# Performance work log

Hardware: AMD Instinct MI355X
Metric: run time of the kernel (lower is better)

## Reference

```python
import jax, jax.numpy as jnp
import numpy as np

N_NODES = 100000
N_EDGES = 1600000
D_IN = 256
D_OUT = 128


def setup_inputs() -> dict:
    key = jax.random.key(0)
    k1, k2, k3, k4, k5, k6 = jax.random.split(key, 6)
    x = jax.random.normal(k1, (N_NODES, D_IN), dtype=jnp.float32)
    W = jax.random.normal(k2, (D_IN, D_OUT), dtype=jnp.float32) * (1.0 / np.sqrt(D_IN))
    b = jax.random.normal(k3, (D_OUT,), dtype=jnp.float32) * 0.01
    edge_row = jax.random.randint(k4, (N_EDGES,), 0, N_NODES, dtype=jnp.int32)
    edge_col = jax.random.randint(k5, (N_EDGES,), 0, N_NODES, dtype=jnp.int32)
    edge_val = jax.random.uniform(k6, (N_EDGES,), dtype=jnp.float32)
    return {"x": x, "W": W, "b": b, "edge_row": edge_row,
            "edge_col": edge_col, "edge_val": edge_val}


def reference(x, W, b, edge_row, edge_col, edge_val):
    # h = Linear(x)  -> [N, D_OUT]
    h = x @ W + b
    # spmm(adj, h): out[i] = sum_{e: row[e]==i} val[e] * h[col[e]]
    msgs = edge_val[:, None] * h[edge_col]          # [E, D_OUT]
    agg = jax.ops.segment_sum(msgs, edge_row, num_segments=N_NODES)
    # activation = relu; dropout=False -> identity
    return jax.nn.relu(agg)
```

## Files before the change

kernel.cpp:

```cpp
#include <hip/hip_runtime.h>

typedef short short8 __attribute__((ext_vector_type(8)));
typedef float f32x4 __attribute__((ext_vector_type(4)));

#define N_NODES 100000
#define N_EDGES 1600000
#define D_IN 256
#define D_OUT 128

#define BROWS 16
#define NBUCK 6250

#define NGRP4 4
#define NCELL4 (NBUCK * NGRP4)
#define NCAP 112
#define C_OFF_H    0UL
#define C_OFF_WP   25600000UL
#define C_OFF_CNT  25665536UL
#define C_OFF_PEV  26065536UL
#define C_WS_NEEDED (C_OFF_PEV + (size_t)NCELL4 * NCAP * 8)

#define NGRP 8
#define NCELL (NBUCK * NGRP)
#define CSTR 4
#define NSB 49
#define OFF_H     0UL
#define OFF_WP    25600000UL
#define OFF_BCNT  25665536UL
#define OFF_BOFF  26465536UL
#define OFF_BS    26665552UL
#define OFF_PEV   26666064UL

__device__ __forceinline__ unsigned short f2bf(float f) {
    unsigned int u = __builtin_bit_cast(unsigned int, f);
    u += 0x7fffu + ((u >> 16) & 1u);
    return (unsigned short)(u >> 16);
}

__global__ void wpack_k(const float* __restrict__ W, unsigned short* __restrict__ wp) {
    int t = blockIdx.x * 256 + threadIdx.x;
    if (t >= 4096) return;
    int ks = t >> 9, nt = (t >> 6) & 7, lane = t & 63;
    int g = lane >> 4, n = nt * 16 + (lane & 15);
    int k0 = ks * 32 + g * 8;
#pragma unroll
    for (int e = 0; e < 8; ++e)
        wp[t * 8 + e] = f2bf(W[(size_t)(k0 + e) * D_OUT + n]);
}

__device__ __forceinline__ void gemm_body(const float* __restrict__ x,
                                          const short8* __restrict__ wq,
                                          const float* __restrict__ b,
                                          unsigned short* __restrict__ h) {
    int wave = threadIdx.x >> 6, lane = threadIdx.x & 63;
    int tile = blockIdx.x * 4 + wave;
    if (tile * 16 >= N_NODES) return;
    int row0 = tile * 16;
    int r = lane & 15, g = lane >> 4;

    f32x4 acc[8];
#pragma unroll
    for (int nt = 0; nt < 8; ++nt)
#pragma unroll
        for (int j = 0; j < 4; ++j) acc[nt][j] = 0.f;

    float bv[8];
#pragma unroll
    for (int nt = 0; nt < 8; ++nt) bv[nt] = b[nt * 16 + r];

    const float4* xp = (const float4*)(x + (size_t)(row0 + r) * D_IN);
#pragma unroll
    for (int ks = 0; ks < 8; ++ks) {
        float4 u0 = xp[ks * 8 + g * 2];
        float4 u1 = xp[ks * 8 + g * 2 + 1];
        short8 af;
        af[0] = (short)f2bf(u0.x); af[1] = (short)f2bf(u0.y);
        af[2] = (short)f2bf(u0.z); af[3] = (short)f2bf(u0.w);
        af[4] = (short)f2bf(u1.x); af[5] = (short)f2bf(u1.y);
        af[6] = (short)f2bf(u1.z); af[7] = (short)f2bf(u1.w);
#pragma unroll
        for (int nt = 0; nt < 8; ++nt) {
            short8 bf = wq[(ks * 8 + nt) * 64 + lane];
            acc[nt] = __builtin_amdgcn_mfma_f32_16x16x32_bf16(af, bf, acc[nt], 0, 0, 0);
        }
    }
#pragma unroll
    for (int nt = 0; nt < 8; ++nt)
#pragma unroll
        for (int j = 0; j < 4; ++j) {
            float v = acc[nt][j] + bv[nt];
            h[(size_t)(row0 + g * 4 + j) * D_OUT + ((nt & 3) * 16 + r) * 2 + (nt >> 2)] = f2bf(v);
        }
}

__global__ __launch_bounds__(256) void gemm_k(const float* __restrict__ x,
                                              const short8* __restrict__ wq,
                                              const float* __restrict__ b,
                                              unsigned short* __restrict__ h) {
    gemm_body(x, wq, b, h);
}

__global__ void binc_k(const int4* __restrict__ er4, const int4* __restrict__ ec4,
                       const float4* __restrict__ ev4,
                       int* __restrict__ cnt, uint2* __restrict__ pev) {
    int t = blockIdx.x * 256 + threadIdx.x;
    int g = blockIdx.x & 3;
    if (t >= N_EDGES / 4) return;
    int4 r = er4[t];
    int4 c = ec4[t];
    float4 v = ev4[t];
    int rows[4] = {r.x, r.y, r.z, r.w};
    int cols[4] = {c.x, c.y, c.z, c.w};
    float vals[4] = {v.x, v.y, v.z, v.w};
    int rel[4], cell[4];
#pragma unroll
    for (int i = 0; i < 4; ++i) {
        cell[i] = (rows[i] >> 4) * NGRP4 + g;
        rel[i] = atomicAdd(&cnt[cell[i] * 4], 1);
    }
#pragma unroll
    for (int i = 0; i < 4; ++i) {
        if (rel[i] < NCAP) {
            uint2 p;
            p.x = (unsigned int)cols[i] | ((unsigned int)(rows[i] & (BROWS - 1)) << 17);
            p.y = __builtin_bit_cast(unsigned int, vals[i]);
            pev[(size_t)cell[i] * NCAP + rel[i]] = p;
        }
    }
}

__device__ __forceinline__ void seg_accum(float* __restrict__ T,
                                          const unsigned int* __restrict__ h32,
                                          const uint2* __restrict__ bpev,
                                          int s, int e, int lane) {
    if (s >= e) return;
    int last = e - 1;
    uint2 pn[8];
#pragma unroll
    for (int j = 0; j < 8; ++j) pn[j] = bpev[min(s + j, last)];
    unsigned int hvc[8];
    float vc[8];
    int rlc[8];
#pragma unroll
    for (int j = 0; j < 8; ++j) {
        hvc[j] = h32[(size_t)(pn[j].x & 0x1FFFFu) * 64 + lane];
        vc[j] = __builtin_bit_cast(float, pn[j].y);
        rlc[j] = (int)(pn[j].x >> 17);
    }
#pragma unroll
    for (int j = 0; j < 8; ++j) pn[j] = bpev[min(s + 8 + j, last)];

    for (int base = s; base < e; base += 8) {
        uint2 pt[8];
#pragma unroll
        for (int j = 0; j < 8; ++j) pt[j] = bpev[min(base + 16 + j, last)];
        unsigned int hvn[8];
        float vn[8];
        int rln[8];
#pragma unroll
        for (int j = 0; j < 8; ++j) {
            hvn[j] = h32[(size_t)(pn[j].x & 0x1FFFFu) * 64 + lane];
            vn[j] = __builtin_bit_cast(float, pn[j].y);
            rln[j] = (int)(pn[j].x >> 17);
        }
#pragma unroll
        for (int j = 0; j < 8; ++j) {
            float v = (base + j < e) ? vc[j] : 0.f;
            float lo = __builtin_bit_cast(float, hvc[j] << 16);
            float hi = __builtin_bit_cast(float, hvc[j] & 0xffff0000u);
            int idx = rlc[j] * 128 + lane;
            float t0 = T[idx], t1 = T[idx + 64];
            T[idx] = fmaf(v, lo, t0);
            T[idx + 64] = fmaf(v, hi, t1);
        }
#pragma unroll
        for (int j = 0; j < 8; ++j) {
            hvc[j] = hvn[j]; vc[j] = vn[j]; rlc[j] = rln[j]; pn[j] = pt[j];
        }
    }
}

__global__ __launch_bounds__(256) void aggc_k(const unsigned int* __restrict__ h32,
                                              const int* __restrict__ cnt,
                                              const uint2* __restrict__ pev,
                                              float* __restrict__ out) {
    __shared__ float tile[4][BROWS * 128];
    int w = threadIdx.x >> 6, lane = threadIdx.x & 63;
    float* T = tile[w];
    int b = blockIdx.x * 4 + w;
    if (b >= NBUCK) return;

    for (int i = lane; i < BROWS * 128 / 4; i += 64) {
        float4 z = {0.f, 0.f, 0.f, 0.f};
        reinterpret_cast<float4*>(T)[i] = z;
    }

#pragma unroll
    for (int g = 0; g < NGRP4; ++g) {
        int cell = b * NGRP4 + g;
        int n = cnt[cell * 4];
        n = (n > NCAP) ? NCAP : n;
        int s = cell * NCAP;
        seg_accum(T, h32, pev, s, s + n, lane);
    }

    int row0 = b * BROWS;
    const float2* T2 = reinterpret_cast<const float2*>(T);
#pragma unroll
    for (int r = 0; r < BROWS; ++r) {
        float2 t2 = T2[r * 64 + lane];
        t2.x = fmaxf(t2.x, 0.f);
        t2.y = fmaxf(t2.y, 0.f);
        reinterpret_cast<float2*>(out + (size_t)(row0 + r) * 128)[lane] = t2;
    }
}

__global__ __launch_bounds__(256) void gemmcnt_k(const float* __restrict__ x,
                                                 const short8* __restrict__ wq,
                                                 const float* __restrict__ b,
                                                 unsigned short* __restrict__ h,
                                                 const int4* __restrict__ er4,
                                                 int* __restrict__ bcnt) {
    int t = blockIdx.x * 256 + threadIdx.x;
    int g0 = blockIdx.x & 7;
    if (t < N_EDGES / 4) {
        int4 r = er4[t];
        atomicAdd(&bcnt[((r.x >> 4) * NGRP + g0) * CSTR], 1);
        atomicAdd(&bcnt[((r.y >> 4) * NGRP + g0) * CSTR], 1);
        atomicAdd(&bcnt[((r.z >> 4) * NGRP + g0) * CSTR], 1);
        atomicAdd(&bcnt[((r.w >> 4) * NGRP + g0) * CSTR], 1);
    }
    gemm_body(x, wq, b, h);
}

__global__ __launch_bounds__(1024) void scan1_k(const int* __restrict__ bcnt,
                                                int* __restrict__ boffs,
                                                int* __restrict__ bs) {
    __shared__ int s[1024];
    int t = threadIdx.x;
    int c = blockIdx.x * 1024 + t;
    int v = (c < NCELL) ? bcnt[c * CSTR] : 0;
    s[t] = v;
    __syncthreads();
    for (int off = 1; off < 1024; off <<= 1) {
        int tmp = (t >= off) ? s[t - off] : 0;
        __syncthreads();
        s[t] += tmp;
        __syncthreads();
    }
    if (c < NCELL) boffs[c] = s[t];
    if (t == 1023) bs[blockIdx.x] = s[1023];
}

__global__ void scan2_k(int* __restrict__ bs, int nb) {
    if (threadIdx.x == 0) {
        int run = 0;
        for (int bb = 0; bb < nb; ++bb) { int t = bs[bb]; bs[bb] = run; run += t; }
        bs[nb] = run;
    }
}

__global__ void scan3_k(int* __restrict__ boffs, int* __restrict__ bcnt,
                        const int* __restrict__ bs) {
    int c = blockIdx.x * 256 + threadIdx.x;
    if (c < NCELL) {
        int v = boffs[c] - bcnt[c * CSTR] + bs[c >> 10];
        boffs[c] = v;
        bcnt[c * CSTR] = v;
    }
    if (c == 0) boffs[NCELL] = bs[NSB];
}

__global__ void bin_k(const int4* __restrict__ er4, const int4* __restrict__ ec4,
                      const float4* __restrict__ ev4,
                      int* __restrict__ bcur, uint2* __restrict__ bpev) {
    int t = blockIdx.x * 256 + threadIdx.x;
    int g = blockIdx.x & 7;
    if (t >= N_EDGES / 4) return;
    int4 r = er4[t];
    int4 c = ec4[t];
    float4 v = ev4[t];
    int rows[4] = {r.x, r.y, r.z, r.w};
    int cols[4] = {c.x, c.y, c.z, c.w};
    float vals[4] = {v.x, v.y, v.z, v.w};
    int pos[4];
#pragma unroll
    for (int i = 0; i < 4; ++i)
        pos[i] = atomicAdd(&bcur[((rows[i] >> 4) * NGRP + g) * CSTR], 1);
#pragma unroll
    for (int i = 0; i < 4; ++i) {
        uint2 p;
        p.x = (unsigned int)cols[i] | ((unsigned int)(rows[i] & (BROWS - 1)) << 17);
        p.y = __builtin_bit_cast(unsigned int, vals[i]);
        bpev[pos[i]] = p;
    }
}

__global__ __launch_bounds__(256) void agg_k(const unsigned int* __restrict__ h32,
                                             const int* __restrict__ boffs,
                                             const uint2* __restrict__ bpev,
                                             float* __restrict__ out) {
    __shared__ float tile[4][BROWS * 128];
    int w = threadIdx.x >> 6, lane = threadIdx.x & 63;
    float* T = tile[w];
    int b = blockIdx.x * 4 + w;
    if (b >= NBUCK) return;

    for (int i = lane; i < BROWS * 128 / 4; i += 64) {
        float4 z = {0.f, 0.f, 0.f, 0.f};
        reinterpret_cast<float4*>(T)[i] = z;
    }
    int s = boffs[b * NGRP], e = boffs[b * NGRP + NGRP];
    seg_accum(T, h32, bpev, s, e, lane);

    int row0 = b * BROWS;
    const float2* T2 = reinterpret_cast<const float2*>(T);
#pragma unroll
    for (int r = 0; r < BROWS; ++r) {
        float2 t2 = T2[r * 64 + lane];
        t2.x = fmaxf(t2.x, 0.f);
        t2.y = fmaxf(t2.y, 0.f);
        reinterpret_cast<float2*>(out + (size_t)(row0 + r) * 128)[lane] = t2;
    }
}

extern "C" void kernel_launch(void* const* d_in, const int* in_sizes, int n_in,
                              void* d_out, int out_size, void* d_ws, size_t ws_size,
                              hipStream_t stream) {
    const float* x = (const float*)d_in[0];
    const float* W = (const float*)d_in[1];
    const float* b = (const float*)d_in[2];
    const int* er = (const int*)d_in[3];
    const int* ec = (const int*)d_in[4];
    const float* ev = (const float*)d_in[5];
    float* out = (float*)d_out;
    char* ws = (char*)d_ws;

    if (ws_size >= C_WS_NEEDED) {
        unsigned short* h = (unsigned short*)(ws + C_OFF_H);
        unsigned short* wp = (unsigned short*)(ws + C_OFF_WP);
        int* cnt = (int*)(ws + C_OFF_CNT);
        uint2* pev = (uint2*)(ws + C_OFF_PEV);

        hipMemsetAsync(cnt, 0, (size_t)NCELL4 * 4 * 4, stream);
        wpack_k<<<16, 256, 0, stream>>>(W, wp);
        gemm_k<<<1563, 256, 0, stream>>>(x, (const short8*)wp, b, h);
        binc_k<<<(N_EDGES / 4 + 255) / 256, 256, 0, stream>>>((const int4*)er, (const int4*)ec,
                                                              (const float4*)ev, cnt, pev);
        aggc_k<<<(NBUCK + 3) / 4, 256, 0, stream>>>((const unsigned int*)h, cnt, pev, out);
    } else {
        unsigned short* h = (unsigned short*)(ws + OFF_H);
        unsigned short* wp = (unsigned short*)(ws + OFF_WP);
        int* bcnt = (int*)(ws + OFF_BCNT);
        int* boffs = (int*)(ws + OFF_BOFF);
        int* bs = (int*)(ws + OFF_BS);
        uint2* bpev = (uint2*)(ws + OFF_PEV);

        hipMemsetAsync(bcnt, 0, (size_t)NCELL * CSTR * 4, stream);
        wpack_k<<<16, 256, 0, stream>>>(W, wp);
        gemmcnt_k<<<1563, 256, 0, stream>>>(x, (const short8*)wp, b, h, (const int4*)er, bcnt);
        scan1_k<<<NSB, 1024, 0, stream>>>(bcnt, boffs, bs);
        scan2_k<<<1, 64, 0, stream>>>(bs, NSB);
        scan3_k<<<(NCELL + 255) / 256, 256, 0, stream>>>(boffs, bcnt, bs);
        bin_k<<<(N_EDGES / 4 + 255) / 256, 256, 0, stream>>>((const int4*)er, (const int4*)ec,
                                                             (const float4*)ev, bcnt, bpev);
        agg_k<<<(NBUCK + 3) / 4, 256, 0, stream>>>((const unsigned int*)h, boffs, bpev, out);
    }
}
```

Before: 216.1 us.

## Pad bin cells to multiples of eight and use scalar edge loads in aggregation

Adds a padfix kernel that rounds each bin cell's count up to a multiple of eight and fills the padding slots with zero-weight edges. This lets the aggregation loop drop per-edge bounds masking. The aggregation kernel now broadcasts each edge's packed index and value through readfirstlane so they live in scalar registers, and it does paired float2 accumulation in LDS. The extra launch and its serialized padding writes add overhead, and padded edges still issue gathers of row 0.

```diff
diff --git a/kernel.cpp b/kernel.cpp
--- a/kernel.cpp
+++ b/kernel.cpp
@@ -129,10 +129,111 @@
     }
 }
 
-__device__ __forceinline__ void seg_accum(float* __restrict__ T,
-                                          const unsigned int* __restrict__ h32,
-                                          const uint2* __restrict__ bpev,
-                                          int s, int e, int lane) {
+__global__ void padfix_k(int* __restrict__ cnt, uint2* __restrict__ pev) {
+    int c = blockIdx.x * 256 + threadIdx.x;
+    if (c >= NCELL4) return;
+    int n = cnt[c * 4];
+    if (n > NCAP) n = NCAP;
+    int n8 = (n + 7) & ~7;
+    uint2 z; z.x = 0u; z.y = 0u;
+    for (int i = n; i < n8; ++i) pev[(size_t)c * NCAP + i] = z;
+    cnt[c * 4] = n8;
+}
+
+__device__ __forceinline__ void seg_accum_pad(float2* __restrict__ T2,
+                                              const unsigned int* __restrict__ h32,
+                                              const uint2* __restrict__ pev,
+                                              int s, int n8, int lane) {
+    if (n8 <= 0) return;
+    int e = s + n8;
+    int last = e - 1;
+
+    uint2 pn[8];
+#pragma unroll
+    for (int j = 0; j < 8; ++j) pn[j] = pev[s + j];
+    unsigned pxc[8]; float pvc[8]; unsigned hvc[8];
+#pragma unroll
+    for (int j = 0; j < 8; ++j) {
+        pxc[j] = (unsigned)__builtin_amdgcn_readfirstlane((int)pn[j].x);
+        pvc[j] = __builtin_bit_cast(float, (unsigned)__builtin_amdgcn_readfirstlane((int)pn[j].y));
+    }
+#pragma unroll
+    for (int j = 0; j < 8; ++j) {
+        const unsigned int* hb = h32 + ((size_t)(pxc[j] & 0x1FFFFu) << 6);
+        hvc[j] = hb[lane];
+    }
+#pragma unroll
+    for (int j = 0; j < 8; ++j) pn[j] = pev[min(s + 8 + j, last)];
+
+    for (int base = s; base < e; base += 8) {
+        uint2 pt[8];
+#pragma unroll
+        for (int j = 0; j < 8; ++j) pt[j] = pev[min(base + 16 + j, last)];
+        unsigned pxn[8]; float pvn[8]; unsigned hvn[8];
+#pragma unroll
+        for (int j = 0; j < 8; ++j) {
+            pxn[j] = (unsigned)__builtin_amdgcn_readfirstlane((int)pn[j].x);
+            pvn[j] = __builtin_bit_cast(float, (unsigned)__builtin_amdgcn_readfirstlane((int)pn[j].y));
+        }
+#pragma unroll
+        for (int j = 0; j < 8; ++j) {
+            const unsigned int* hb = h32 + ((size_t)(pxn[j] & 0x1FFFFu) << 6);
+            hvn[j] = hb[lane];
+        }
+#pragma unroll
+        for (int j = 0; j < 8; ++j) {
+            float v = pvc[j];
+            float lo = __builtin_bit_cast(float, hvc[j] << 16);
+            float hi = __builtin_bit_cast(float, hvc[j] & 0xffff0000u);
+            int idx2 = (int)(pxc[j] >> 17) * 64 + lane;
+            float2 t = T2[idx2];
+            t.x = fmaf(v, lo, t.x);
+            t.y = fmaf(v, hi, t.y);
+            T2[idx2] = t;
+        }
+#pragma unroll
+        for (int j = 0; j < 8; ++j) {
+            hvc[j] = hvn[j]; pxc[j] = pxn[j]; pvc[j] = pvn[j]; pn[j] = pt[j];
+        }
+    }
+}
+
+__global__ __launch_bounds__(256) void aggc_k(const unsigned int* __restrict__ h32,
+                                              const int* __restrict__ cnt,
+                                              const uint2* __restrict__ pev,
+                                              float* __restrict__ out) {
+    __shared__ float2 tile[4][BROWS * 64];
+    int w = threadIdx.x >> 6, lane = threadIdx.x & 63;
+    float2* T2 = tile[w];
+    int b = blockIdx.x * 4 + w;
+    if (b >= NBUCK) return;
+
+    float4* T4 = reinterpret_cast<float4*>(T2);
+    for (int i = lane; i < BROWS * 32; i += 64) {
+        float4 z = {0.f, 0.f, 0.f, 0.f};
+        T4[i] = z;
+    }
+
+#pragma unroll
+    for (int g = 0; g < NGRP4; ++g) {
+        int cell = b * NGRP4 + g;
+        int n8 = cnt[cell * 4];
+        seg_accum_pad(T2, h32, pev, cell * NCAP, n8, lane);
+    }
+
+    int row0 = b * BROWS;
+#pragma unroll
+    for (int r = 0; r < BROWS; ++r) {
+        float2 t2 = T2[r * 64 + lane];
+        out[(size_t)(row0 + r) * 128 + lane]      = fmaxf(t2.x, 0.f);
+        out[(size_t)(row0 + r) * 128 + 64 + lane] = fmaxf(t2.y, 0.f);
+    }
+}
+
+__device__ __forceinline__ void seg_accum_legacy(float* __restrict__ T,
+                                                 const unsigned int* __restrict__ h32,
+                                                 const uint2* __restrict__ bpev,
+                                                 int s, int e, int lane) {
     if (s >= e) return;
     int last = e - 1;
     uint2 pn[8];
@@ -177,41 +278,6 @@
         for (int j = 0; j < 8; ++j) {
             hvc[j] = hvn[j]; vc[j] = vn[j]; rlc[j] = rln[j]; pn[j] = pt[j];
         }
-    }
-}
-
-__global__ __launch_bounds__(256) void aggc_k(const unsigned int* __restrict__ h32,
-                                              const int* __restrict__ cnt,
-                                              const uint2* __restrict__ pev,
-                                              float* __restrict__ out) {
-    __shared__ float tile[4][BROWS * 128];
-    int w = threadIdx.x >> 6, lane = threadIdx.x & 63;
-    float* T = tile[w];
-    int b = blockIdx.x * 4 + w;
-    if (b >= NBUCK) return;
-
-    for (int i = lane; i < BROWS * 128 / 4; i += 64) {
-        float4 z = {0.f, 0.f, 0.f, 0.f};
-        reinterpret_cast<float4*>(T)[i] = z;
-    }
-
-#pragma unroll
-    for (int g = 0; g < NGRP4; ++g) {
-        int cell = b * NGRP4 + g;
-        int n = cnt[cell * 4];
-        n = (n > NCAP) ? NCAP : n;
-        int s = cell * NCAP;
-        seg_accum(T, h32, pev, s, s + n, lane);
-    }
-
-    int row0 = b * BROWS;
-    const float2* T2 = reinterpret_cast<const float2*>(T);
-#pragma unroll
-    for (int r = 0; r < BROWS; ++r) {
-        float2 t2 = T2[r * 64 + lane];
-        t2.x = fmaxf(t2.x, 0.f);
-        t2.y = fmaxf(t2.y, 0.f);
-        reinterpret_cast<float2*>(out + (size_t)(row0 + r) * 128)[lane] = t2;
     }
 }
 
@@ -311,7 +377,7 @@
         reinterpret_cast<float4*>(T)[i] = z;
     }
     int s = boffs[b * NGRP], e = boffs[b * NGRP + NGRP];
-    seg_accum(T, h32, bpev, s, e, lane);
+    seg_accum_legacy(T, h32, bpev, s, e, lane);
 
     int row0 = b * BROWS;
     const float2* T2 = reinterpret_cast<const float2*>(T);
@@ -347,6 +413,7 @@
         gemm_k<<<1563, 256, 0, stream>>>(x, (const short8*)wp, b, h);
         binc_k<<<(N_EDGES / 4 + 255) / 256, 256, 0, stream>>>((const int4*)er, (const int4*)ec,
                                                               (const float4*)ev, cnt, pev);
+        padfix_k<<<(NCELL4 + 255) / 256, 256, 0, stream>>>(cnt, pev);
         aggc_k<<<(NBUCK + 3) / 4, 256, 0, stream>>>((const unsigned int*)h, cnt, pev, out);
     } else {
         unsigned short* h = (unsigned short*)(ws + OFF_H);
```

New measurement: 224.4 us. 1.04x slower.
